# Performance work log

Measured on AMD Instinct MI355X. Metric: run time of the kernel, lower is better.

The kernel has to match this reference:

```python
import jax, jax.numpy as jnp
import numpy as np
import math

D_MODEL = 2048
NUM_HEADS = 16
D_K = D_MODEL // NUM_HEADS  # 128
SEQ_LEN = 2048
THETA = 10000.0
BATCH = 2


def setup_inputs() -> dict:
    key = jax.random.key(0)
    ks = jax.random.split(key, 5)
    std = (2.0 / (D_MODEL + D_MODEL)) ** 0.5
    return {
        "x": jax.random.normal(ks[0], (BATCH, SEQ_LEN, D_MODEL), dtype=jnp.float32),
        "Wq": jax.random.normal(ks[1], (D_MODEL, D_MODEL), dtype=jnp.float32) * std,
        "Wk": jax.random.normal(ks[2], (D_MODEL, D_MODEL), dtype=jnp.float32) * std,
        "Wv": jax.random.normal(ks[3], (D_MODEL, D_MODEL), dtype=jnp.float32) * std,
        "Wo": jax.random.normal(ks[4], (D_MODEL, D_MODEL), dtype=jnp.float32) * std,
    }


def _rope(t):
    # t: [B, H, S, d_k]; apply rotary embedding on interleaved even/odd pairs
    S = t.shape[-2]
    dk = t.shape[-1]
    inv_freq = jnp.exp(-math.log(THETA) * jnp.arange(0, dk, 2, dtype=jnp.float32) / dk)  # [dk/2]
    pos = jnp.arange(S, dtype=jnp.float32)
    freqs = pos[:, None] * inv_freq[None, :]  # [S, dk/2]
    cos = jnp.cos(freqs)
    sin = jnp.sin(freqs)
    t1 = t[..., ::2]   # [B, H, S, dk/2]
    t2 = t[..., 1::2]
    rot = jnp.stack([t1 * cos - t2 * sin, t1 * sin + t2 * cos], axis=-1)  # [B,H,S,dk/2,2]
    return rot.reshape(t.shape)


def reference(x, Wq, Wk, Wv, Wo):
    B, S, D = x.shape
    H, dk = NUM_HEADS, D // NUM_HEADS

    def split_heads(t):
        return t.reshape(B, S, H, dk).transpose(0, 2, 1, 3)  # [B,H,S,dk]

    q = split_heads(x @ Wq.T)
    k = split_heads(x @ Wk.T)
    v = split_heads(x @ Wv.T)

    q = _rope(q)
    k = _rope(k)

    scores = jnp.einsum("bhqd,bhkd->bhqk", q, k) / math.sqrt(dk)  # [B,H,S,S]
    causal = jnp.tril(jnp.ones((S, S), dtype=bool))
    scores = jnp.where(causal[None, None], scores, -jnp.inf)
    attn = jax.nn.softmax(scores, axis=-1)
    ctx = jnp.einsum("bhqk,bhkd->bhqd", attn, v)  # [B,H,S,dk]
    ctx = ctx.transpose(0, 2, 1, 3).reshape(B, S, D)
    return ctx @ Wo.T
```

## Files before the change

kernel.cpp:

```cpp
#include <hip/hip_runtime.h>
#include <stdint.h>
#include <type_traits>

#define S_LEN 2048
#define DM 2048
#define NH 16
#define DKH 128
#define NB 2
#define NROWS (NB * S_LEN)

typedef unsigned short u16;
typedef __attribute__((ext_vector_type(8))) __bf16 bf16x8;
typedef __attribute__((ext_vector_type(4))) float f32x4;

__device__ __forceinline__ float bf2f(u16 u) {
  union { unsigned u; float f; } v; v.u = ((unsigned)u) << 16; return v.f;
}
__device__ __forceinline__ u16 f2bf(float f) {
  union { float f; unsigned u; } v; v.f = f;
  unsigned r = v.u + 0x7FFFu + ((v.u >> 16) & 1u);
  return (u16)(r >> 16);
}

__device__ __forceinline__ void async_copy16(void* lds, const void* g) {
  __builtin_amdgcn_global_load_lds(
      (const __attribute__((address_space(1))) unsigned int*)g,
      (__attribute__((address_space(3))) unsigned int*)lds, 16, 0, 0);
}

__global__ void cast_all_kernel(const float* __restrict__ x, const float* __restrict__ wq,
                                const float* __restrict__ wk, const float* __restrict__ wv,
                                const float* __restrict__ wo, u16* __restrict__ xb,
                                u16* __restrict__ wqkv, u16* __restrict__ wob) {
  const int XN4 = NROWS * DM / 4;
  const int WN4 = DM * DM / 4;
  int total = XN4 + 4 * WN4;
  int stride = gridDim.x * blockDim.x;
  for (int i = blockIdx.x * blockDim.x + threadIdx.x; i < total; i += stride) {
    const float* s;
    u16* d;
    int j;
    if (i < XN4) {
      s = x; d = xb; j = i;
    } else {
      int k = i - XN4;
      int w = k >> 20;
      j = k & 0xFFFFF;
      if (w == 0) { s = wq; d = wqkv; }
      else if (w == 1) { s = wk; d = wqkv + (size_t)DM * DM; }
      else if (w == 2) { s = wv; d = wqkv + (size_t)2 * DM * DM; }
      else { s = wo; d = wob; }
    }
    float4 v = ((const float4*)s)[j];
    unsigned r0 = (unsigned)f2bf(v.x) | ((unsigned)f2bf(v.y) << 16);
    unsigned r1 = (unsigned)f2bf(v.z) | ((unsigned)f2bf(v.w) << 16);
    ((uint2*)d)[j] = make_uint2(r0, r1);
  }
}

__global__ void rope_table_kernel(float2* __restrict__ ctab) {
  int idx = blockIdx.x * blockDim.x + threadIdx.x;
  if (idx >= S_LEN * 64) return;
  int s = idx >> 6, i = idx & 63;
  float inv = expf(-9.210340371976184f * (float)i * (1.0f / 64.0f));
  float fr = (float)s * inv;
  ctab[idx] = make_float2(cosf(fr), sinf(fr));
}

template <int NSEG, int EPI>
__global__ __launch_bounds__(512, 1) void gemm256_kernel(const u16* __restrict__ A,
                                                         const u16* __restrict__ B,
                                                         void* __restrict__ C0,
                                                         void* __restrict__ C1,
                                                         void* __restrict__ C2,
                                                         const float2* __restrict__ ctab,
                                                         int M, int N, int Kd) {
  constexpr int BN = 64 * NSEG;
  constexpr int BSZ = BN * 128;
  constexpr int LDS_AE = 0, LDS_AO = 32768, LDS_BE = 65536, LDS_BO = 65536 + BSZ;

  extern __shared__ char smem[];
  u16* lds = (u16*)smem;

  int tid = threadIdx.x;
  int lane = tid & 63, wave = tid >> 6;
  int lr = lane & 15, lg = lane >> 4;
  int wm = wave >> 2, wn = wave & 3;

  int gx = gridDim.x, nwg = gx * gridDim.y;
  int bid = blockIdx.y * gx + blockIdx.x;
  int cpx = nwg >> 3;
  int swz = (bid & 7) * cpx + (bid >> 3);
  int tm = (swz / gx) * 256, tn = (swz % gx) * BN;

  int srow_in = lane >> 3;
  int scolb = ((lane & 7) * 16) ^ ((lane >> 3) << 4);

  const u16* Arows = A + (size_t)tm * Kd;
  const u16* Brows = B + (size_t)tn * Kd;

  auto stageA = [&](int aBase, int h, int kt) {
#pragma unroll
    for (int l = 0; l < 2; l++) {
      int ch = h * 16 + l * 8 + wave;
      async_copy16(lds + ((aBase + ch * 1024) >> 1),
                   Arows + (size_t)(ch * 8 + srow_in) * Kd + kt * 64 + (scolb >> 1));
    }
  };
  auto stageB = [&](int bBase, int s, int kt) {
    int ch = s * 8 + wave;
    async_copy16(lds + ((bBase + ch * 1024) >> 1),
                 Brows + (size_t)(ch * 8 + srow_in) * Kd + kt * 64 + (scolb >> 1));
  };

  int acolb[2];
#pragma unroll
  for (int ks = 0; ks < 2; ks++) acolb[ks] = (ks * 64 + lg * 16) ^ ((lr & 7) << 4);
  int aBaseW = wm * 128 * 128;
  int brow_b = (wn * 16 * NSEG + lr) * 128;

  f32x4 zero4 = {0.f, 0.f, 0.f, 0.f};
  f32x4 acc[8][NSEG];
#pragma unroll
  for (int i = 0; i < 8; i++)
#pragma unroll
    for (int j = 0; j < NSEG; j++) acc[i][j] = zero4;

  bf16x8 bpre[NSEG][2];
  bf16x8 af[2][2];

  auto loadB = [&](int bBase) {
#pragma unroll
    for (int nf = 0; nf < NSEG; nf++)
#pragma unroll
      for (int ks = 0; ks < 2; ks++)
        bpre[nf][ks] = *(const bf16x8*)&lds[(bBase + brow_b + nf * 2048 + acolb[ks]) >> 1];
  };
  auto readA = [&](int aBase, int q) {
#pragma unroll
    for (int dm = 0; dm < 2; dm++)
#pragma unroll
      for (int ks = 0; ks < 2; ks++)
        af[dm][ks] = *(const bf16x8*)&lds[(aBase + aBaseW + (2 * q + dm) * 2048 + lr * 128 +
                                           acolb[ks]) >> 1];
  };
  auto mfmaC = [&](auto qc) {
    constexpr int Q = decltype(qc)::value;
    __builtin_amdgcn_s_setprio(1);
#pragma unroll
    for (int dm = 0; dm < 2; dm++)
#pragma unroll
      for (int nf = 0; nf < NSEG; nf++)
#pragma unroll
        for (int ks = 0; ks < 2; ks++)
          acc[2 * Q + dm][nf] = __builtin_amdgcn_mfma_f32_16x16x32_bf16(
              af[dm][ks], bpre[nf][ks], acc[2 * Q + dm][nf], 0, 0, 0);
    __builtin_amdgcn_s_setprio(0);
  };
  auto bar_pre = [&]() {
    __builtin_amdgcn_s_barrier();
    asm volatile("s_waitcnt lgkmcnt(0)" ::: "memory");
    __builtin_amdgcn_sched_barrier(0);
  };
  auto vm_wait = [&]() {
    if constexpr (NSEG == 3) asm volatile("s_waitcnt vmcnt(3)" ::: "memory");
    else asm volatile("s_waitcnt vmcnt(2)" ::: "memory");
  };

  int nk = Kd >> 6;
  int nIter = nk >> 1;

  stageA(LDS_AE, 0, 0);
  stageA(LDS_AE, 1, 0);
#pragma unroll
  for (int s = 0; s < NSEG; s++) stageB(LDS_BE, s, 0);
#pragma unroll
  for (int s = 0; s < NSEG; s++) stageB(LDS_BO, s, 1);
  vm_wait();
  __builtin_amdgcn_s_barrier();

  for (int i = 0; i < nIter; i++) {
    int tO = 2 * i + 1;
    int tE2 = 2 * i + 2; if (tE2 > nk - 1) tE2 = nk - 1;
    int tO2 = 2 * i + 3; if (tO2 > nk - 1) tO2 = nk - 1;

    loadB(LDS_BE); readA(LDS_AE, 0);
    stageA(LDS_AO, 0, tO);
    asm volatile("s_waitcnt lgkmcnt(8)" ::: "memory");
    bar_pre();
    mfmaC(std::integral_constant<int, 0>{});
    __builtin_amdgcn_s_barrier();
    readA(LDS_AE, 1);
    stageA(LDS_AO, 1, tO);
    bar_pre();
    mfmaC(std::integral_constant<int, 1>{});
    __builtin_amdgcn_s_barrier();
    readA(LDS_AE, 2);
    stageB(LDS_BE, 0, tE2);
    if constexpr (NSEG == 3) stageB(LDS_BE, 1, tE2);
    bar_pre();
    mfmaC(std::integral_constant<int, 2>{});
    __builtin_amdgcn_s_barrier();
    readA(LDS_AE, 3);
    stageB(LDS_BE, NSEG - 1, tE2);
    vm_wait();
    bar_pre();
    mfmaC(std::integral_constant<int, 3>{});
    __builtin_amdgcn_s_barrier();
    loadB(LDS_BO); readA(LDS_AO, 0);
    stageA(LDS_AE, 0, tE2);
    asm volatile("s_waitcnt lgkmcnt(8)" ::: "memory");
    bar_pre();
    mfmaC(std::integral_constant<int, 0>{});
    __builtin_amdgcn_s_barrier();
    readA(LDS_AO, 1);
    stageA(LDS_AE, 1, tE2);
    bar_pre();
    mfmaC(std::integral_constant<int, 1>{});
    __builtin_amdgcn_s_barrier();
    readA(LDS_AO, 2);
    stageB(LDS_BO, 0, tO2);
    if constexpr (NSEG == 3) stageB(LDS_BO, 1, tO2);
    bar_pre();
    mfmaC(std::integral_constant<int, 2>{});
    __builtin_amdgcn_s_barrier();
    readA(LDS_AO, 3);
    stageB(LDS_BO, NSEG - 1, tO2);
    vm_wait();
    bar_pre();
    mfmaC(std::integral_constant<int, 3>{});
    __builtin_amdgcn_s_barrier();
  }

  asm volatile("s_waitcnt vmcnt(0)" ::: "memory");

#pragma unroll
  for (int mf = 0; mf < 8; mf++) {
    int row = tm + wm * 128 + mf * 16 + lg * 4;
#pragma unroll
    for (int nf = 0; nf < NSEG; nf++) {
      int col = tn + wn * 16 * NSEG + nf * 16 + lr;
      if constexpr (EPI == 0) {
        float* O = (float*)C0;
#pragma unroll
        for (int r = 0; r < 4; r++) O[(size_t)(row + r) * N + col] = acc[mf][nf][r];
      } else {
        int mat = col >> 11, lc = col & 2047;
        if (mat < 2) {
          u16* O = (mat == 0) ? (u16*)C0 : (u16*)C1;
          int d = lc & 127;
          bool odd = (d & 1) != 0;
          const float2* ct = ctab + (d >> 1);
#pragma unroll
          for (int r = 0; r < 4; r++) {
            float a = acc[mf][nf][r];
            float pp = __shfl_xor(a, 1);
            int sIdx = (row + r) & (S_LEN - 1);
            float2 cs = ct[sIdx * 64];
            float o = odd ? (pp * cs.y + a * cs.x) : (a * cs.x - pp * cs.y);
            O[(size_t)(row + r) * 2048 + lc] = f2bf(o);
          }
        } else {
          u16* O = (u16*)C2;
          int h = lc >> 7, d = lc & 127;
          int bb = row >> 11, s0 = row & 2047;
          unsigned w0 = (unsigned)f2bf(acc[mf][nf][0]) | ((unsigned)f2bf(acc[mf][nf][1]) << 16);
          unsigned w1 = (unsigned)f2bf(acc[mf][nf][2]) | ((unsigned)f2bf(acc[mf][nf][3]) << 16);
          *(uint2*)(O + ((size_t)((bb * 16 + h) * 128 + d) * 2048 + s0)) = make_uint2(w0, w1);
        }
      }
    }
  }
}

__device__ __forceinline__ int kidx(int row, int colb) {
  return ((row << 8) + (colb ^ ((row & 7) << 4))) >> 1;
}
__device__ __forceinline__ int vidx(int row, int colb) {
  return ((row << 7) + (colb ^ ((row & 7) << 4))) >> 1;
}

__global__ __launch_bounds__(256, 2) void attn_kernel(const u16* __restrict__ Q,
                                                      const u16* __restrict__ K,
                                                      const u16* __restrict__ Vt,
                                                      u16* __restrict__ ctx) {
  __shared__ u16 Kl[2][64 * 128];
  __shared__ u16 Vl[2][128 * 64];

  int tid = threadIdx.x;
  int lane = tid & 63, wave = tid >> 6;
  int lr = lane & 15, lg = lane >> 4;
  int bh = blockIdx.x;
  int b = bh >> 4, h = bh & 15;
  int p = blockIdx.y;
  int half = blockIdx.z;
  int q0s = p * 128 + half * 64 + wave * 16;
  int q0b = (15 - p) * 128 + half * 64 + wave * 16;

  bf16x8 qf[2][4];
#pragma unroll
  for (int mf = 0; mf < 2; mf++) {
    int base = mf ? q0b : q0s;
    const u16* qbase = Q + (size_t)(b * S_LEN + base + lr) * DM + h * DKH;
#pragma unroll
    for (int ks = 0; ks < 4; ks++) qf[mf][ks] = *(const bf16x8*)(qbase + ks * 32 + lg * 8);
  }

  f32x4 zero4 = {0.f, 0.f, 0.f, 0.f};
  f32x4 acc[2][8];
#pragma unroll
  for (int mf = 0; mf < 2; mf++)
#pragma unroll
    for (int f = 0; f < 8; f++) acc[mf][f] = zero4;
  float m_r[2], l_r[2];
#pragma unroll
  for (int mf = 0; mf < 2; mf++) { m_r[mf] = -3.0e38f; l_r[mf] = 0.f; }

  const float SL2E = 1.4426950408889634f * 0.08838834764831845f;
  const float RTHR = 64.0f;

  const u16* Kbh = K + (size_t)b * S_LEN * DM + h * DKH;
  const u16* Vbh = Vt + (size_t)(b * NH + h) * DKH * S_LEN;

  auto stage = [&](int buf, int kv0s) {
#pragma unroll
    for (int c = 0; c < 4; c++) {
      int ch = wave * 4 + c;
      int krow = ch * 4 + (lane >> 4);
      int kphi = (krow & 0x23) | ((krow & 0x10) >> 2) | ((krow & 0x0C) << 1);
      int kcb = ((((lane & 15) << 4) ^ ((krow & 7) << 4)) >> 1);
      async_copy16(&Kl[buf][ch * 512], Kbh + (size_t)(kv0s + kphi) * DM + kcb);
      int vrow = ch * 8 + (lane >> 3);
      int vcb = ((((lane & 7) << 4) ^ ((vrow & 7) << 4)) >> 1);
      async_copy16(&Vl[buf][ch * 512], Vbh + (size_t)vrow * S_LEN + kv0s + vcb);
    }
  };

  auto tileCompute = [&](int kv0, int bufIdx, auto nMfC) {
    constexpr int NMF = decltype(nMfC)::value;
    f32x4 sf[4][NMF];
#pragma unroll
    for (int kf = 0; kf < 4; kf++)
#pragma unroll
      for (int mi = 0; mi < NMF; mi++) sf[kf][mi] = zero4;
    __builtin_amdgcn_s_setprio(1);
#pragma unroll
    for (int ks = 0; ks < 4; ks++)
#pragma unroll
      for (int kf = 0; kf < 4; kf++) {
        bf16x8 kfrag = *(const bf16x8*)&Kl[bufIdx][kidx(kf * 16 + lr, ks * 64 + lg * 16)];
#pragma unroll
        for (int mi = 0; mi < NMF; mi++) {
          int mf = (NMF == 2) ? mi : 1;
          sf[kf][mi] = __builtin_amdgcn_mfma_f32_16x16x32_bf16(kfrag, qf[mf][ks], sf[kf][mi], 0, 0, 0);
        }
      }
    __builtin_amdgcn_s_setprio(0);

    float sv[NMF][4][4];
    float mx[NMF];
#pragma unroll
    for (int mi = 0; mi < NMF; mi++) {
      int mf = (NMF == 2) ? mi : 1;
      int base = mf ? q0b : q0s;
      int qg = base + lr;
      bool need_mask = (kv0 + 63 > base);
      mx[mi] = -3.0e38f;
#pragma unroll
      for (int kf = 0; kf < 4; kf++) {
        int kvb = kv0 + (kf >> 1) * 32 + (kf & 1) * 4 + lg * 8;
#pragma unroll
        for (int r = 0; r < 4; r++) {
          float x = sf[kf][mi][r];
          if (need_mask) x = (kvb + r <= qg) ? x : -3.0e38f;
          sv[mi][kf][r] = x;
          mx[mi] = fmaxf(mx[mi], x);
        }
      }
      mx[mi] = fmaxf(mx[mi], __shfl_xor(mx[mi], 16));
      mx[mi] = fmaxf(mx[mi], __shfl_xor(mx[mi], 32));
    }

    bool need = false;
#pragma unroll
    for (int mi = 0; mi < NMF; mi++) {
      int mf = (NMF == 2) ? mi : 1;
      need = need | (mx[mi] > m_r[mf] + RTHR);
    }
    if (__any(need)) {
      float scs[NMF];
#pragma unroll
      for (int mi = 0; mi < NMF; mi++) {
        int mf = (NMF == 2) ? mi : 1;
        float mnew = fmaxf(m_r[mf], mx[mi]);
        scs[mi] = __builtin_amdgcn_exp2f((m_r[mf] - mnew) * SL2E);
        m_r[mf] = mnew;
        l_r[mf] *= scs[mi];
      }
#pragma unroll
      for (int mi = 0; mi < NMF; mi++) {
        int mf = (NMF == 2) ? mi : 1;
#pragma unroll
        for (int r = 0; r < 4; r++) {
          float sa = __shfl(scs[mi], (lane & 0x30) | (lg * 4 + r));
#pragma unroll
          for (int f = 0; f < 8; f++) acc[mf][f][r] *= sa;
        }
      }
    }

    bf16x8 pf[NMF][2];
#pragma unroll
    for (int mi = 0; mi < NMF; mi++) {
      int mf = (NMF == 2) ? mi : 1;
      float rs = 0.f;
#pragma unroll
      for (int kf = 0; kf < 4; kf++)
#pragma unroll
        for (int r = 0; r < 4; r++) {
          float pv = __builtin_amdgcn_exp2f((sv[mi][kf][r] - m_r[mf]) * SL2E);
          sv[mi][kf][r] = pv;
          rs += pv;
        }
      rs += __shfl_xor(rs, 16);
      rs += __shfl_xor(rs, 32);
      l_r[mf] += rs;
#pragma unroll
      for (int ks2 = 0; ks2 < 2; ks2++) {
        bf16x8 t2;
#pragma unroll
        for (int r = 0; r < 4; r++) {
          t2[r] = (__bf16)sv[mi][2 * ks2][r];
          t2[4 + r] = (__bf16)sv[mi][2 * ks2 + 1][r];
        }
        pf[mi][ks2] = t2;
      }
    }

    __builtin_amdgcn_s_setprio(1);
#pragma unroll
    for (int ks2 = 0; ks2 < 2; ks2++)
#pragma unroll
      for (int f = 0; f < 8; f++) {
        bf16x8 vf = *(const bf16x8*)&Vl[bufIdx][vidx(f * 16 + lr, ks2 * 64 + lg * 16)];
#pragma unroll
        for (int mi = 0; mi < NMF; mi++) {
          int mf = (NMF == 2) ? mi : 1;
          acc[mf][f] = __builtin_amdgcn_mfma_f32_16x16x32_bf16(pf[mi][ks2], vf, acc[mf][f], 0, 0, 0);
        }
      }
    __builtin_amdgcn_s_setprio(0);
  };

  int ntB = 2 * (15 - p) + 2;
  stage(0, 0);
  int cur = 0;

  for (int t = 0; t < ntB; t++) {
    int kv0 = t * 64;
    if (t + 1 < ntB) {
      stage(cur ^ 1, (t + 1) * 64);
      asm volatile("s_waitcnt vmcnt(8)" ::: "memory");
    } else {
      asm volatile("s_waitcnt vmcnt(0)" ::: "memory");
    }
    asm volatile("s_barrier" ::: "memory");
    __builtin_amdgcn_sched_barrier(0);

    bool actS = (kv0 <= q0s + 15);
    bool actB = (kv0 <= q0b + 15);
    if (actS) tileCompute(kv0, cur, std::integral_constant<int, 2>{});
    else if (actB) tileCompute(kv0, cur, std::integral_constant<int, 1>{});

    asm volatile("s_barrier" ::: "memory");
    cur ^= 1;
  }

#pragma unroll
  for (int mf = 0; mf < 2; mf++) {
    int base = mf ? q0b : q0s;
    float invl = 1.0f / l_r[mf];
#pragma unroll
    for (int r = 0; r < 4; r++) {
      float ia = __shfl(invl, (lane & 0x30) | (lg * 4 + r));
      int rowg = b * S_LEN + base + lg * 4 + r;
#pragma unroll
      for (int f = 0; f < 8; f++) {
        int colg = h * DKH + f * 16 + lr;
        ctx[(size_t)rowg * DM + colg] = f2bf(acc[mf][f][r] * ia);
      }
    }
  }
}

extern "C" void kernel_launch(void* const* d_in, const int* in_sizes, int n_in,
                              void* d_out, int out_size, void* d_ws, size_t ws_size,
                              hipStream_t stream) {
  const float* x = (const float*)d_in[0];
  const float* Wq = (const float*)d_in[1];
  const float* Wk = (const float*)d_in[2];
  const float* Wv = (const float*)d_in[3];
  const float* Wo = (const float*)d_in[4];
  float* out = (float*)d_out;

  char* ws = (char*)d_ws;
  size_t off = 0;
  auto alloc = [&](size_t bytes) -> char* {
    char* p = ws + off;
    off += (bytes + 255) & ~(size_t)255;
    return p;
  };
  u16* xb = (u16*)alloc((size_t)NROWS * DM * 2);
  u16* wqkv = (u16*)alloc((size_t)3 * DM * DM * 2);
  u16* wob = (u16*)alloc((size_t)DM * DM * 2);
  u16* Qb = (u16*)alloc((size_t)NROWS * DM * 2);
  u16* Kb = (u16*)alloc((size_t)NROWS * DM * 2);
  u16* Vtb = (u16*)alloc((size_t)NROWS * DM * 2);
  float2* ctab = (float2*)alloc((size_t)S_LEN * 64 * 8);
  u16* ctx = xb;

  hipFuncSetAttribute((const void*)gemm256_kernel<3, 2>,
                      hipFuncAttributeMaxDynamicSharedMemorySize, 65536 + 2 * 192 * 128);
  hipFuncSetAttribute((const void*)gemm256_kernel<2, 0>,
                      hipFuncAttributeMaxDynamicSharedMemorySize, 65536 + 2 * 128 * 128);

  cast_all_kernel<<<2048, 256, 0, stream>>>(x, Wq, Wk, Wv, Wo, xb, wqkv, wob);
  rope_table_kernel<<<(S_LEN * 64 + 255) / 256, 256, 0, stream>>>(ctab);

  gemm256_kernel<3, 2><<<dim3(3 * DM / 192, NROWS / 256), 512, 65536 + 2 * 192 * 128, stream>>>(
      xb, wqkv, Qb, Kb, Vtb, ctab, NROWS, 3 * DM, DM);

  attn_kernel<<<dim3(NB * NH, 8, 2), 256, 0, stream>>>(Qb, Kb, Vtb, ctx);

  gemm256_kernel<2, 0><<<dim3(DM / 128, NROWS / 256), 512, 65536 + 2 * 128 * 128, stream>>>(
      ctx, wob, out, nullptr, nullptr, nullptr, NROWS, DM, DM);
}
```

Before: 238.9 us.

## Move RoPE out of QKV GEMM epilogue into a separate vectorized kernel

Removes the RoPE rotation from the QKV GEMM epilogue. The epilogue now writes Q/K as packed bf16 pairs, with even lanes storing 32-bit words, and V-transpose stores widened to 16 bytes via lane shuffles. A new grid-stride kernel then re-reads Q and K, applies the rotation using float4 cos/sin loads, and writes them back in place. This aims to cut the epilogue's scattered per-element table loads and narrow stores, but adds a full extra read and write pass over Q and K plus one more launch.

```diff
diff --git a/kernel.cpp b/kernel.cpp
--- a/kernel.cpp
+++ b/kernel.cpp
@@ -67,13 +67,38 @@
   ctab[idx] = make_float2(cosf(fr), sinf(fr));
 }
 
+__global__ void rope2_kernel(u16* __restrict__ Q, u16* __restrict__ K,
+                             const float2* __restrict__ ctab) {
+  const int NP = NROWS * 512;
+  int total = 2 * NP;
+  int stride = gridDim.x * blockDim.x;
+  for (int p = blockIdx.x * blockDim.x + threadIdx.x; p < total; p += stride) {
+    u16* T = (p < NP) ? Q : K;
+    int j = (p < NP) ? p : p - NP;
+    int row = j >> 9;
+    int t = j & 511;
+    int i0 = (2 * t) & 63;
+    int s = row & (S_LEN - 1);
+    u16* addr = T + ((size_t)row * DM + 4 * t);
+    uint2 v = *(uint2*)addr;
+    float4 cs4 = *(const float4*)&ctab[s * 64 + i0];
+    float a0 = bf2f((u16)(v.x & 0xffff)), b0 = bf2f((u16)(v.x >> 16));
+    float a1 = bf2f((u16)(v.y & 0xffff)), b1 = bf2f((u16)(v.y >> 16));
+    float o0 = a0 * cs4.x - b0 * cs4.y, o1 = a0 * cs4.y + b0 * cs4.x;
+    float o2 = a1 * cs4.z - b1 * cs4.w, o3 = a1 * cs4.w + b1 * cs4.z;
+    uint2 w;
+    w.x = (unsigned)f2bf(o0) | ((unsigned)f2bf(o1) << 16);
+    w.y = (unsigned)f2bf(o2) | ((unsigned)f2bf(o3) << 16);
+    *(uint2*)addr = w;
+  }
+}
+
 template <int NSEG, int EPI>
 __global__ __launch_bounds__(512, 1) void gemm256_kernel(const u16* __restrict__ A,
                                                          const u16* __restrict__ B,
                                                          void* __restrict__ C0,
                                                          void* __restrict__ C1,
                                                          void* __restrict__ C2,
-                                                         const float2* __restrict__ ctab,
                                                          int M, int N, int Kd) {
   constexpr int BN = 64 * NSEG;
   constexpr int BSZ = BN * 128;
@@ -248,17 +273,14 @@
         int mat = col >> 11, lc = col & 2047;
         if (mat < 2) {
           u16* O = (mat == 0) ? (u16*)C0 : (u16*)C1;
-          int d = lc & 127;
-          bool odd = (d & 1) != 0;
-          const float2* ct = ctab + (d >> 1);
 #pragma unroll
           for (int r = 0; r < 4; r++) {
             float a = acc[mf][nf][r];
-            float pp = __shfl_xor(a, 1);
-            int sIdx = (row + r) & (S_LEN - 1);
-            float2 cs = ct[sIdx * 64];
-            float o = odd ? (pp * cs.y + a * cs.x) : (a * cs.x - pp * cs.y);
-            O[(size_t)(row + r) * 2048 + lc] = f2bf(o);
+            float b = __shfl_xor(a, 1);
+            if (!(lr & 1)) {
+              unsigned w = (unsigned)f2bf(a) | ((unsigned)f2bf(b) << 16);
+              *(unsigned*)(O + (size_t)(row + r) * 2048 + lc) = w;
+            }
           }
         } else {
           u16* O = (u16*)C2;
@@ -266,7 +288,12 @@
           int bb = row >> 11, s0 = row & 2047;
           unsigned w0 = (unsigned)f2bf(acc[mf][nf][0]) | ((unsigned)f2bf(acc[mf][nf][1]) << 16);
           unsigned w1 = (unsigned)f2bf(acc[mf][nf][2]) | ((unsigned)f2bf(acc[mf][nf][3]) << 16);
-          *(uint2*)(O + ((size_t)((bb * 16 + h) * 128 + d) * 2048 + s0)) = make_uint2(w0, w1);
+          unsigned w0p = __shfl_xor(w0, 16);
+          unsigned w1p = __shfl_xor(w1, 16);
+          if (!(lg & 1)) {
+            *(uint4*)(O + ((size_t)((bb * 16 + h) * 128 + d) * 2048 + s0)) =
+                make_uint4(w0, w1, w0p, w1p);
+          }
         }
       }
     }
@@ -528,10 +555,12 @@
   rope_table_kernel<<<(S_LEN * 64 + 255) / 256, 256, 0, stream>>>(ctab);
 
   gemm256_kernel<3, 2><<<dim3(3 * DM / 192, NROWS / 256), 512, 65536 + 2 * 192 * 128, stream>>>(
-      xb, wqkv, Qb, Kb, Vtb, ctab, NROWS, 3 * DM, DM);
+      xb, wqkv, Qb, Kb, Vtb, NROWS, 3 * DM, DM);
+
+  rope2_kernel<<<2048, 256, 0, stream>>>(Qb, Kb, ctab);
 
   attn_kernel<<<dim3(NB * NH, 8, 2), 256, 0, stream>>>(Qb, Kb, Vtb, ctx);
 
   gemm256_kernel<2, 0><<<dim3(DM / 128, NROWS / 256), 512, 65536 + 2 * 128 * 128, stream>>>(
-      ctx, wob, out, nullptr, nullptr, nullptr, NROWS, DM, DM);
-}
+      ctx, wob, out, nullptr, nullptr, NROWS, DM, DM);
+}
```

Result: slower. 248.2 us (+3.9%).

## Move Q RoPE into attention, widen QKV epilogue stores, remap QKV tile order

Applied to the files above, without the earlier changes.

Q is now stored unrotated by the QKV GEMM and RoPE is applied to Q fragments after they are loaded in the attention kernel, which removes the table lookup from the GEMM epilogue. The Q, K and Vt epilogue stores are widened by exchanging values across lanes with shuffles, so each store writes 32 or 128 bits instead of scattered 16-bit or 64-bit writes. The QKV GEMM also gets a hard-coded block-to-tile mapping meant to improve L2 reuse. The cost is extra shuffles, half the lanes sitting idle during stores, and rotating Q in bf16 after rounding, which slightly changes numerics.

```diff
diff --git a/kernel.cpp b/kernel.cpp
--- a/kernel.cpp
+++ b/kernel.cpp
@@ -89,9 +89,18 @@
 
   int gx = gridDim.x, nwg = gx * gridDim.y;
   int bid = blockIdx.y * gx + blockIdx.x;
-  int cpx = nwg >> 3;
-  int swz = (bid & 7) * cpx + (bid >> 3);
-  int tm = (swz / gx) * 256, tn = (swz % gx) * BN;
+  int tmI, tnI;
+  if constexpr (EPI == 2) {
+    int k = bid & 7, j = bid >> 3;
+    tmI = j & 15;
+    tnI = k * 4 + (j >> 4);
+  } else {
+    int cpx = nwg >> 3;
+    int swz = (bid & 7) * cpx + (bid >> 3);
+    tmI = swz / gx;
+    tnI = swz % gx;
+  }
+  int tm = tmI * 256, tn = tnI * BN;
 
   int srow_in = lane >> 3;
   int scolb = ((lane & 7) * 16) ^ ((lane >> 3) << 4);
@@ -246,8 +255,19 @@
         for (int r = 0; r < 4; r++) O[(size_t)(row + r) * N + col] = acc[mf][nf][r];
       } else {
         int mat = col >> 11, lc = col & 2047;
-        if (mat < 2) {
-          u16* O = (mat == 0) ? (u16*)C0 : (u16*)C1;
+        if (mat == 0) {
+          u16* O = (u16*)C0;
+#pragma unroll
+          for (int r = 0; r < 4; r++) {
+            float a = acc[mf][nf][r];
+            float b = __shfl_xor(a, 1);
+            if (!(lr & 1)) {
+              unsigned w = (unsigned)f2bf(a) | ((unsigned)f2bf(b) << 16);
+              *(unsigned*)(O + (size_t)(row + r) * 2048 + lc) = w;
+            }
+          }
+        } else if (mat == 1) {
+          u16* O = (u16*)C1;
           int d = lc & 127;
           bool odd = (d & 1) != 0;
           const float2* ct = ctab + (d >> 1);
@@ -255,10 +275,13 @@
           for (int r = 0; r < 4; r++) {
             float a = acc[mf][nf][r];
             float pp = __shfl_xor(a, 1);
-            int sIdx = (row + r) & (S_LEN - 1);
-            float2 cs = ct[sIdx * 64];
+            float2 cs = ct[((row + r) & (S_LEN - 1)) * 64];
             float o = odd ? (pp * cs.y + a * cs.x) : (a * cs.x - pp * cs.y);
-            O[(size_t)(row + r) * 2048 + lc] = f2bf(o);
+            float ob = __shfl_xor(o, 1);
+            if (!(lr & 1)) {
+              unsigned w = (unsigned)f2bf(o) | ((unsigned)f2bf(ob) << 16);
+              *(unsigned*)(O + (size_t)(row + r) * 2048 + lc) = w;
+            }
           }
         } else {
           u16* O = (u16*)C2;
@@ -266,7 +289,12 @@
           int bb = row >> 11, s0 = row & 2047;
           unsigned w0 = (unsigned)f2bf(acc[mf][nf][0]) | ((unsigned)f2bf(acc[mf][nf][1]) << 16);
           unsigned w1 = (unsigned)f2bf(acc[mf][nf][2]) | ((unsigned)f2bf(acc[mf][nf][3]) << 16);
-          *(uint2*)(O + ((size_t)((bb * 16 + h) * 128 + d) * 2048 + s0)) = make_uint2(w0, w1);
+          unsigned w0p = __shfl_xor(w0, 16);
+          unsigned w1p = __shfl_xor(w1, 16);
+          if (!(lg & 1)) {
+            *(uint4*)(O + ((size_t)((bb * 16 + h) * 128 + d) * 2048 + s0)) =
+                make_uint4(w0, w1, w0p, w1p);
+          }
         }
       }
     }
@@ -283,6 +311,7 @@
 __global__ __launch_bounds__(256, 2) void attn_kernel(const u16* __restrict__ Q,
                                                       const u16* __restrict__ K,
                                                       const u16* __restrict__ Vt,
+                                                      const float2* __restrict__ ctab,
                                                       u16* __restrict__ ctx) {
   __shared__ u16 Kl[2][64 * 128];
   __shared__ u16 Vl[2][128 * 64];
@@ -305,6 +334,25 @@
 #pragma unroll
     for (int ks = 0; ks < 4; ks++) qf[mf][ks] = *(const bf16x8*)(qbase + ks * 32 + lg * 8);
   }
+#pragma unroll
+  for (int mf = 0; mf < 2; mf++) {
+    int base = mf ? q0b : q0s;
+    const float2* ct = ctab + (size_t)(base + lr) * 64;
+#pragma unroll
+    for (int ks = 0; ks < 4; ks++) {
+      bf16x8 q = qf[mf][ks];
+      bf16x8 o;
+      int i0 = ks * 16 + lg * 4;
+#pragma unroll
+      for (int pr = 0; pr < 4; pr++) {
+        float2 cs = ct[i0 + pr];
+        float a = (float)q[2 * pr], bb2 = (float)q[2 * pr + 1];
+        o[2 * pr] = (__bf16)(a * cs.x - bb2 * cs.y);
+        o[2 * pr + 1] = (__bf16)(a * cs.y + bb2 * cs.x);
+      }
+      qf[mf][ks] = o;
+    }
+  }
 
   f32x4 zero4 = {0.f, 0.f, 0.f, 0.f};
   f32x4 acc[2][8];
@@ -530,7 +578,7 @@
   gemm256_kernel<3, 2><<<dim3(3 * DM / 192, NROWS / 256), 512, 65536 + 2 * 192 * 128, stream>>>(
       xb, wqkv, Qb, Kb, Vtb, ctab, NROWS, 3 * DM, DM);
 
-  attn_kernel<<<dim3(NB * NH, 8, 2), 256, 0, stream>>>(Qb, Kb, Vtb, ctx);
+  attn_kernel<<<dim3(NB * NH, 8, 2), 256, 0, stream>>>(Qb, Kb, Vtb, ctab, ctx);
 
   gemm256_kernel<2, 0><<<dim3(DM / 128, NROWS / 256), 512, 65536 + 2 * 128 * 128, stream>>>(
       ctx, wob, out, nullptr, nullptr, nullptr, NROWS, DM, DM);
```

Measured after the change: 266.9 us. 11.7% more time.
